# Performance work log

Hardware: AMD Instinct MI355X
Metric: run time of the kernel (lower is better)

## Reference

```python
import jax, jax.numpy as jnp
import numpy as np

LAMBD = 1.0  # margin, matches init kwarg lambd
N, C, D = 16384, 4096, 128


def setup_inputs() -> dict:
    key = jax.random.key(0)
    k1, k2, k3 = jax.random.split(key, 3)
    embeddings = jax.random.normal(k1, (N, D), dtype=jnp.float32)
    targets = jax.random.randint(k2, (N,), 0, C, dtype=jnp.int64)
    centers = jax.random.normal(k3, (C, D), dtype=jnp.float32)
    return {"embeddings": embeddings, "targets": targets, "centers": centers}


def reference(embeddings, targets, centers):
    # Squared euclidean distances from every sample to every center, [n, C],
    # via ||e||^2 + ||c||^2 - 2 e.c (avoids the [n, C, d] broadcast tensor).
    e2 = jnp.sum(embeddings * embeddings, axis=-1, keepdims=True)          # [n, 1]
    c2 = jnp.sum(centers * centers, axis=-1)                               # [C]
    dist = e2 + c2[None, :] - 2.0 * jnp.matmul(embeddings, centers.T)      # [n, C]

    tgt = targets.astype(jnp.int32)
    ap = jnp.take_along_axis(dist, tgt[:, None], axis=1)                   # [n, 1]

    # loss_val[i, c] = lambd + d(e_i, center_{y_i}) - d(e_i, center_c)
    loss_val = LAMBD + ap - dist                                           # [n, C]

    # Triplet (i, y_i, c) is mined iff loss_val > 0 and c != y_i.
    not_label = jnp.arange(dist.shape[1], dtype=jnp.int32)[None, :] != tgt[:, None]
    mask = (loss_val > 0.0) & not_label

    # For mined triplets relu(ap - an + lambd) == loss_val (already > 0).
    total = jnp.sum(jnp.where(mask, loss_val, 0.0))
    cnt = jnp.sum(mask).astype(loss_val.dtype)
    # If no triplet violates the margin, the original returns 0.
    return jnp.where(cnt > 0.0, total / jnp.maximum(cnt, 1.0), 0.0)
```

## Files before the change

kernel.cpp:

```cpp
#include <hip/hip_runtime.h>

#define N_SAMP 16384
#define N_CENT 4096
#define DIM    128
#define LAMBD  1.0f
#define NSLOT  256

typedef _Float16 half8  __attribute__((ext_vector_type(8)));
typedef float    floatx4 __attribute__((ext_vector_type(4)));

struct Slot { float sum; unsigned int cnt; unsigned int pad[30]; };

__device__ __forceinline__ void gload_lds16(const void* g, void* l) {
  __builtin_amdgcn_global_load_lds(
      (__attribute__((address_space(1))) void*)(g),
      (__attribute__((address_space(3))) void*)(l), 16, 0, 0);
}

__global__ __launch_bounds__(256) void prep_kernel(
    const float* __restrict__ E, const float* __restrict__ Cc,
    const int* __restrict__ tgt,
    _Float16* __restrict__ Eh, _Float16* __restrict__ Ch,
    float* __restrict__ c2, float* __restrict__ rowk,
    Slot* __restrict__ slots) {
  const int tid = threadIdx.x;
  const int STAT_BLOCKS = (N_SAMP + N_CENT) / 4;
  if ((int)blockIdx.x < STAT_BLOCKS) {
    if (blockIdx.x == 0) { slots[tid].sum = 0.f; slots[tid].cnt = 0u; }
    const int wv   = blockIdx.x * 4 + (tid >> 6);
    const int lane = tid & 63;
    if (wv < N_SAMP) {
      const int yi = tgt[wv];
      float2 e = *(const float2*)(E  + (size_t)wv * DIM + lane * 2);
      float2 c = *(const float2*)(Cc + (size_t)yi * DIM + lane * 2);
      float s = c.x * (c.x - 2.f * e.x) + c.y * (c.y - 2.f * e.y);
      #pragma unroll
      for (int off = 32; off > 0; off >>= 1) s += __shfl_down(s, off);
      if (lane == 0) rowk[wv] = LAMBD + s;
    } else {
      const int cI = wv - N_SAMP;
      float2 c = *(const float2*)(Cc + (size_t)cI * DIM + lane * 2);
      float s = c.x * c.x + c.y * c.y;
      #pragma unroll
      for (int off = 32; off > 0; off >>= 1) s += __shfl_down(s, off);
      if (lane == 0) c2[cI] = s;
    }
  } else {
    const int t = ((int)blockIdx.x - STAT_BLOCKS) * 256 + tid;
    const int NE8 = N_SAMP * DIM / 8;
    const float4* src;
    half8* dst;
    int idx;
    if (t < NE8) { src = (const float4*)E;  dst = (half8*)Eh; idx = t; }
    else         { src = (const float4*)Cc; dst = (half8*)Ch; idx = t - NE8; }
    float4 a = src[(size_t)idx * 2], b = src[(size_t)idx * 2 + 1];
    half8 h;
    h[0]=(_Float16)a.x; h[1]=(_Float16)a.y; h[2]=(_Float16)a.z; h[3]=(_Float16)a.w;
    h[4]=(_Float16)b.x; h[5]=(_Float16)b.y; h[6]=(_Float16)b.z; h[7]=(_Float16)b.w;
    dst[idx] = h;
  }
}

__global__ __launch_bounds__(256, 2) void center_gemm_kernel(
    const _Float16* __restrict__ Eh, const _Float16* __restrict__ Ch,
    const float* __restrict__ c2, const float* __restrict__ rowk,
    const int* __restrict__ tgt,
    Slot* __restrict__ slots) {
  __shared__ _Float16 As[128 * DIM];
  __shared__ _Float16 Bs[128 * DIM];
  __shared__ float rowkS[128];
  __shared__ float c2S[128];
  __shared__ int   yS[128];
  __shared__ float swsum[4];
  __shared__ int   swcnt[4];

  const int tid  = threadIdx.x;
  const int w    = tid >> 6;
  const int lane = tid & 63;

  const int bid = blockIdx.x;
  const int xcd = bid & 7;
  const int j   = bid >> 3;
  const int bm  = xcd * 16 + (j & 15);
  const int bn  = j >> 4;

  {
    const char* gA = (const char*)(Eh + (size_t)bm * 128 * DIM);
    const char* gB = (const char*)(Ch + (size_t)bn * 128 * DIM);
    char* lA = (char*)As;
    char* lB = (char*)Bs;
    const int p  = lane & 15;
    const int r4 = lane >> 4;
    #pragma unroll
    for (int it = 0; it < 8; ++it) {
      const int off = (w * 8 + it) * 1024;
      const int row = (w * 8 + it) * 4 + r4;
      const int gof = row * 256 + (p ^ (row & 15)) * 16;
      gload_lds16(gA + gof, lA + off);
      gload_lds16(gB + gof, lB + off);
    }
  }
  if (tid < 128) {
    rowkS[tid] = rowk[bm * 128 + tid];
    yS[tid]    = tgt[bm * 128 + tid];
    c2S[tid]   = c2[bn * 128 + tid];
  }
  __syncthreads();

  const int wm = w >> 1, wn = w & 1;
  const int q = lane >> 4, r = lane & 15;
  const int row0 = wm * 64, col0 = wn * 64;

  floatx4 acc[4][4];
  #pragma unroll
  for (int a = 0; a < 4; ++a)
    #pragma unroll
    for (int b = 0; b < 4; ++b)
      acc[a][b] = (floatx4){0.f, 0.f, 0.f, 0.f};

  #pragma unroll
  for (int ks = 0; ks < 4; ++ks) {
    const int cidx = ks * 4 + q;
    half8 af[4], bf[4];
    #pragma unroll
    for (int mt = 0; mt < 4; ++mt)
      af[mt] = *(const half8*)&As[(row0 + mt * 16 + r) * DIM + ((cidx ^ r) * 8)];
    #pragma unroll
    for (int nt = 0; nt < 4; ++nt)
      bf[nt] = *(const half8*)&Bs[(col0 + nt * 16 + r) * DIM + ((cidx ^ r) * 8)];
    #pragma unroll
    for (int mt = 0; mt < 4; ++mt)
      #pragma unroll
      for (int nt = 0; nt < 4; ++nt)
        acc[mt][nt] = __builtin_amdgcn_mfma_f32_16x16x32_f16(af[mt], bf[nt], acc[mt][nt], 0, 0, 0);
  }

  float lsum = 0.f;
  int   lcnt = 0;
  #pragma unroll
  for (int mt = 0; mt < 4; ++mt) {
    float rk[4]; int yv[4];
    #pragma unroll
    for (int rg = 0; rg < 4; ++rg) {
      const int row = row0 + mt * 16 + q * 4 + rg;
      rk[rg] = rowkS[row];
      yv[rg] = yS[row];
    }
    #pragma unroll
    for (int nt = 0; nt < 4; ++nt) {
      const int col  = col0 + nt * 16 + r;
      const float c2v = c2S[col];
      const int gcol = bn * 128 + col;
      #pragma unroll
      for (int rg = 0; rg < 4; ++rg) {
        const float v = rk[rg] + 2.f * acc[mt][nt][rg] - c2v;
        const bool mined = (v > 0.f) & (gcol != yv[rg]);
        lsum += mined ? v : 0.f;
        lcnt += mined ? 1 : 0;
      }
    }
  }

  #pragma unroll
  for (int off = 32; off > 0; off >>= 1) {
    lsum += __shfl_down(lsum, off);
    lcnt += __shfl_down(lcnt, off);
  }
  if (lane == 0) { swsum[w] = lsum; swcnt[w] = lcnt; }
  __syncthreads();
  if (tid == 0) {
    const float s = swsum[0] + swsum[1] + swsum[2] + swsum[3];
    const int   c = swcnt[0] + swcnt[1] + swcnt[2] + swcnt[3];
    Slot* sl = &slots[bid & (NSLOT - 1)];
    atomicAdd(&sl->sum, s);
    atomicAdd(&sl->cnt, (unsigned int)c);
  }
}

__global__ __launch_bounds__(256) void finalize_kernel(
    const Slot* __restrict__ slots, float* __restrict__ out) {
  const int tid = threadIdx.x;
  float s = slots[tid].sum;
  unsigned int c = slots[tid].cnt;
  #pragma unroll
  for (int off = 32; off > 0; off >>= 1) {
    s += __shfl_down(s, off);
    c += __shfl_down(c, off);
  }
  __shared__ float ss[4];
  __shared__ unsigned int sc[4];
  if ((tid & 63) == 0) { ss[tid >> 6] = s; sc[tid >> 6] = c; }
  __syncthreads();
  if (tid == 0) {
    const float S = ss[0] + ss[1] + ss[2] + ss[3];
    const unsigned int C = sc[0] + sc[1] + sc[2] + sc[3];
    out[0] = (C > 0u) ? (S / (float)C) : 0.f;
  }
}

__global__ void zero_kernel(float* ws_sum, unsigned int* ws_cnt) {
  if (threadIdx.x == 0) { *ws_sum = 0.f; *ws_cnt = 0u; }
}

__global__ void finalize_simple(const float* __restrict__ ws_sum,
                                const unsigned int* __restrict__ ws_cnt,
                                float* __restrict__ out) {
  if (threadIdx.x == 0 && blockIdx.x == 0) {
    const unsigned int c = *ws_cnt;
    out[0] = (c > 0u) ? (*ws_sum / (float)c) : 0.f;
  }
}

__global__ __launch_bounds__(256) void fallback_kernel(
    const float* __restrict__ E, const float* __restrict__ Cc,
    const int* __restrict__ tgt,
    float* __restrict__ ws_sum, unsigned int* __restrict__ ws_cnt) {
  __shared__ float eS[DIM];
  __shared__ float apS;
  const int i = blockIdx.x;
  const int tid = threadIdx.x;
  if (tid < DIM) eS[tid] = E[(size_t)i * DIM + tid];
  __syncthreads();
  const int yi = tgt[i];
  float dloc[16];
  #pragma unroll
  for (int j = 0; j < 16; ++j) {
    const int c = tid + 256 * j;
    const float* cp = Cc + (size_t)c * DIM;
    float s = 0.f;
    for (int d = 0; d < DIM; d += 4) {
      float4 cv = *(const float4*)(cp + d);
      s += cv.x * (cv.x - 2.f * eS[d + 0]) + cv.y * (cv.y - 2.f * eS[d + 1])
         + cv.z * (cv.z - 2.f * eS[d + 2]) + cv.w * (cv.w - 2.f * eS[d + 3]);
    }
    dloc[j] = s;
    if (c == yi) apS = s;
  }
  __syncthreads();
  const float apv = apS;
  float lsum = 0.f; int lcnt = 0;
  #pragma unroll
  for (int j = 0; j < 16; ++j) {
    const int c = tid + 256 * j;
    const float v = LAMBD + apv - dloc[j];
    const bool mined = (v > 0.f) & (c != yi);
    lsum += mined ? v : 0.f;
    lcnt += mined ? 1 : 0;
  }
  #pragma unroll
  for (int off = 32; off > 0; off >>= 1) {
    lsum += __shfl_down(lsum, off);
    lcnt += __shfl_down(lcnt, off);
  }
  __shared__ float swsum[4];
  __shared__ int   swcnt[4];
  const int w = tid >> 6, lane = tid & 63;
  if (lane == 0) { swsum[w] = lsum; swcnt[w] = lcnt; }
  __syncthreads();
  if (tid == 0) {
    atomicAdd(ws_sum, swsum[0] + swsum[1] + swsum[2] + swsum[3]);
    atomicAdd(ws_cnt, (unsigned int)(swcnt[0] + swcnt[1] + swcnt[2] + swcnt[3]));
  }
}

extern "C" void kernel_launch(void* const* d_in, const int* in_sizes, int n_in,
                              void* d_out, int out_size, void* d_ws, size_t ws_size,
                              hipStream_t stream) {
  const float* E   = (const float*)d_in[0];
  const int*   tgt = (const int*)d_in[1];
  const float* Cc  = (const float*)d_in[2];
  float* out = (float*)d_out;

  const size_t EH_BYTES = (size_t)N_SAMP * DIM * 2;
  const size_t CH_BYTES = (size_t)N_CENT * DIM * 2;
  const size_t C2_BYTES = (size_t)N_CENT * 4;
  const size_t RK_BYTES = (size_t)N_SAMP * 4;
  const size_t SL_BYTES = (size_t)NSLOT * sizeof(Slot);
  const size_t NEEDED = EH_BYTES + CH_BYTES + C2_BYTES + RK_BYTES + SL_BYTES;

  char* ws = (char*)d_ws;
  if (ws_size >= NEEDED) {
    _Float16* Eh = (_Float16*)ws;
    _Float16* Ch = (_Float16*)(ws + EH_BYTES);
    float* c2    = (float*)(ws + EH_BYTES + CH_BYTES);
    float* rowk  = (float*)(ws + EH_BYTES + CH_BYTES + C2_BYTES);
    Slot* slots  = (Slot*)(ws + EH_BYTES + CH_BYTES + C2_BYTES + RK_BYTES);

    const int STAT_BLOCKS = (N_SAMP + N_CENT) / 4;
    const int CONV_BLOCKS = (N_SAMP * DIM / 8 + N_CENT * DIM / 8) / 256;
    prep_kernel<<<STAT_BLOCKS + CONV_BLOCKS, 256, 0, stream>>>(
        E, Cc, tgt, Eh, Ch, c2, rowk, slots);
    center_gemm_kernel<<<(N_CENT / 128) * (N_SAMP / 128), 256, 0, stream>>>(
        Eh, Ch, c2, rowk, tgt, slots);
    finalize_kernel<<<1, 256, 0, stream>>>(slots, out);
  } else {
    float* ws_sum = (float*)ws;
    unsigned int* ws_cnt = (unsigned int*)(ws_sum + 1);
    zero_kernel<<<1, 64, 0, stream>>>(ws_sum, ws_cnt);
    fallback_kernel<<<N_SAMP, 256, 0, stream>>>(E, Cc, tgt, ws_sum, ws_cnt);
    finalize_simple<<<1, 64, 0, stream>>>(ws_sum, ws_cnt, out);
  }
}
```

Before: 100.5 us.

## Load A fragments straight to registers, drop A LDS tile, raise occupancy

The GEMM kernel no longer stages the embedding tile in LDS. Each wave loads its A fragments directly from global memory into registers, which halves LDS use per block and allows launch bounds of 3 blocks per SIMD. The prep kernel's row-stat path now uses 16 lanes per row with float4 loads instead of a full wave per row. The direct global loads of A are less coalesced and add register pressure, which could cause spills at the higher occupancy target.

Result: slower. 104.9 us (+4.4%).

```diff
diff --git a/kernel.cpp b/kernel.cpp
--- a/kernel.cpp
+++ b/kernel.cpp
@@ -24,26 +24,36 @@
     float* __restrict__ c2, float* __restrict__ rowk,
     Slot* __restrict__ slots) {
   const int tid = threadIdx.x;
-  const int STAT_BLOCKS = (N_SAMP + N_CENT) / 4;
+  const int STAT_BLOCKS = (N_SAMP + N_CENT) / 16;
   if ((int)blockIdx.x < STAT_BLOCKS) {
     if (blockIdx.x == 0) { slots[tid].sum = 0.f; slots[tid].cnt = 0u; }
-    const int wv   = blockIdx.x * 4 + (tid >> 6);
-    const int lane = tid & 63;
-    if (wv < N_SAMP) {
-      const int yi = tgt[wv];
-      float2 e = *(const float2*)(E  + (size_t)wv * DIM + lane * 2);
-      float2 c = *(const float2*)(Cc + (size_t)yi * DIM + lane * 2);
-      float s = c.x * (c.x - 2.f * e.x) + c.y * (c.y - 2.f * e.y);
-      #pragma unroll
-      for (int off = 32; off > 0; off >>= 1) s += __shfl_down(s, off);
-      if (lane == 0) rowk[wv] = LAMBD + s;
+    const int row   = blockIdx.x * 16 + (tid >> 4);
+    const int l16   = tid & 15;
+    if (row < N_SAMP) {
+      const int yi = tgt[row];
+      const float4* e = (const float4*)(E  + (size_t)row * DIM + l16 * 8);
+      const float4* c = (const float4*)(Cc + (size_t)yi  * DIM + l16 * 8);
+      float4 e0 = e[0], e1 = e[1], c0 = c[0], c1 = c[1];
+      float s = c0.x*(c0.x-2.f*e0.x) + c0.y*(c0.y-2.f*e0.y)
+              + c0.z*(c0.z-2.f*e0.z) + c0.w*(c0.w-2.f*e0.w)
+              + c1.x*(c1.x-2.f*e1.x) + c1.y*(c1.y-2.f*e1.y)
+              + c1.z*(c1.z-2.f*e1.z) + c1.w*(c1.w-2.f*e1.w);
+      s += __shfl_down(s, 8, 16);
+      s += __shfl_down(s, 4, 16);
+      s += __shfl_down(s, 2, 16);
+      s += __shfl_down(s, 1, 16);
+      if (l16 == 0) rowk[row] = LAMBD + s;
     } else {
-      const int cI = wv - N_SAMP;
-      float2 c = *(const float2*)(Cc + (size_t)cI * DIM + lane * 2);
-      float s = c.x * c.x + c.y * c.y;
-      #pragma unroll
-      for (int off = 32; off > 0; off >>= 1) s += __shfl_down(s, off);
-      if (lane == 0) c2[cI] = s;
+      const int cI = row - N_SAMP;
+      const float4* c = (const float4*)(Cc + (size_t)cI * DIM + l16 * 8);
+      float4 c0 = c[0], c1 = c[1];
+      float s = c0.x*c0.x + c0.y*c0.y + c0.z*c0.z + c0.w*c0.w
+              + c1.x*c1.x + c1.y*c1.y + c1.z*c1.z + c1.w*c1.w;
+      s += __shfl_down(s, 8, 16);
+      s += __shfl_down(s, 4, 16);
+      s += __shfl_down(s, 2, 16);
+      s += __shfl_down(s, 1, 16);
+      if (l16 == 0) c2[cI] = s;
     }
   } else {
     const int t = ((int)blockIdx.x - STAT_BLOCKS) * 256 + tid;
@@ -61,12 +71,11 @@
   }
 }
 
-__global__ __launch_bounds__(256, 2) void center_gemm_kernel(
+__global__ __launch_bounds__(256, 3) void center_gemm_kernel(
     const _Float16* __restrict__ Eh, const _Float16* __restrict__ Ch,
     const float* __restrict__ c2, const float* __restrict__ rowk,
     const int* __restrict__ tgt,
     Slot* __restrict__ slots) {
-  __shared__ _Float16 As[128 * DIM];
   __shared__ _Float16 Bs[128 * DIM];
   __shared__ float rowkS[128];
   __shared__ float c2S[128];
@@ -77,6 +86,7 @@
   const int tid  = threadIdx.x;
   const int w    = tid >> 6;
   const int lane = tid & 63;
+  const int q = lane >> 4, r = lane & 15;
 
   const int bid = blockIdx.x;
   const int xcd = bid & 7;
@@ -85,9 +95,7 @@
   const int bn  = j >> 4;
 
   {
-    const char* gA = (const char*)(Eh + (size_t)bm * 128 * DIM);
     const char* gB = (const char*)(Ch + (size_t)bn * 128 * DIM);
-    char* lA = (char*)As;
     char* lB = (char*)Bs;
     const int p  = lane & 15;
     const int r4 = lane >> 4;
@@ -96,10 +104,20 @@
       const int off = (w * 8 + it) * 1024;
       const int row = (w * 8 + it) * 4 + r4;
       const int gof = row * 256 + (p ^ (row & 15)) * 16;
-      gload_lds16(gA + gof, lA + off);
       gload_lds16(gB + gof, lB + off);
     }
   }
+
+  const int wm = w >> 1, wn = w & 1;
+  const int row0 = wm * 64, col0 = wn * 64;
+  half8 areg[4][4];
+  #pragma unroll
+  for (int ks = 0; ks < 4; ++ks)
+    #pragma unroll
+    for (int mt = 0; mt < 4; ++mt)
+      areg[ks][mt] = *(const half8*)&Eh[
+          (size_t)(bm * 128 + row0 + mt * 16 + r) * DIM + ks * 32 + q * 8];
+
   if (tid < 128) {
     rowkS[tid] = rowk[bm * 128 + tid];
     yS[tid]    = tgt[bm * 128 + tid];
@@ -107,10 +125,6 @@
   }
   __syncthreads();
 
-  const int wm = w >> 1, wn = w & 1;
-  const int q = lane >> 4, r = lane & 15;
-  const int row0 = wm * 64, col0 = wn * 64;
-
   floatx4 acc[4][4];
   #pragma unroll
   for (int a = 0; a < 4; ++a)
@@ -121,10 +135,7 @@
   #pragma unroll
   for (int ks = 0; ks < 4; ++ks) {
     const int cidx = ks * 4 + q;
-    half8 af[4], bf[4];
-    #pragma unroll
-    for (int mt = 0; mt < 4; ++mt)
-      af[mt] = *(const half8*)&As[(row0 + mt * 16 + r) * DIM + ((cidx ^ r) * 8)];
+    half8 bf[4];
     #pragma unroll
     for (int nt = 0; nt < 4; ++nt)
       bf[nt] = *(const half8*)&Bs[(col0 + nt * 16 + r) * DIM + ((cidx ^ r) * 8)];
@@ -132,7 +143,7 @@
     for (int mt = 0; mt < 4; ++mt)
       #pragma unroll
       for (int nt = 0; nt < 4; ++nt)
-        acc[mt][nt] = __builtin_amdgcn_mfma_f32_16x16x32_f16(af[mt], bf[nt], acc[mt][nt], 0, 0, 0);
+        acc[mt][nt] = __builtin_amdgcn_mfma_f32_16x16x32_f16(areg[ks][mt], bf[nt], acc[mt][nt], 0, 0, 0);
   }
 
   float lsum = 0.f;
@@ -286,7 +297,7 @@
     float* rowk  = (float*)(ws + EH_BYTES + CH_BYTES + C2_BYTES);
     Slot* slots  = (Slot*)(ws + EH_BYTES + CH_BYTES + C2_BYTES + RK_BYTES);
 
-    const int STAT_BLOCKS = (N_SAMP + N_CENT) / 4;
+    const int STAT_BLOCKS = (N_SAMP + N_CENT) / 16;
     const int CONV_BLOCKS = (N_SAMP * DIM / 8 + N_CENT * DIM / 8) / 256;
     prep_kernel<<<STAT_BLOCKS + CONV_BLOCKS, 256, 0, stream>>>(
         E, Cc, tgt, Eh, Ch, c2, rowk, slots);
```
